# Kernel tuning notes

Hardware: AMD Instinct MI355X
Metric: run time of the kernel (lower is better)

The kernel has to match this reference:

```python
import jax, jax.numpy as jnp
import numpy as np

N_USER = 50000
N_ITEM = 100000
D = 64            # embed_size; layer_size = [64, 64, 64]
NL = 3            # number of propagation layers
NNZ = 2400000     # nonzeros of sparse Laplacian L
B = 1024          # batch of (user, pos_item, neg_item)
N = N_USER + N_ITEM


def setup_inputs() -> dict:
    key = jax.random.key(0)
    ks = jax.random.split(key, 20)
    inp = {}
    # learned parameters
    inp["user_emb"] = jax.random.normal(ks[0], (N_USER, D), jnp.float32) * 0.1
    inp["item_emb"] = jax.random.normal(ks[1], (N_ITEM, D), jnp.float32) * 0.1
    inp["lin1_w"] = jax.random.normal(ks[2], (4, D // 2), jnp.float32) * 0.5
    inp["lin1_b"] = jnp.zeros((D // 2,), jnp.float32)
    inp["lin2_w"] = jax.random.normal(ks[3], (D // 2, D), jnp.float32) * 0.2
    inp["lin2_b"] = jnp.zeros((D,), jnp.float32)
    inp["w1"] = jax.random.normal(ks[4], (NL, D, D), jnp.float32) * (1.0 / np.sqrt(D))
    inp["b1"] = jnp.zeros((NL, D), jnp.float32)
    inp["w2"] = jax.random.normal(ks[5], (NL, D, D), jnp.float32) * (1.0 / np.sqrt(D))
    inp["b2"] = jnp.zeros((NL, D), jnp.float32)
    # sparse normalized Laplacian L in COO form (eye_mat handled as +E)
    inp["lap_row"] = jax.random.randint(ks[6], (NNZ,), 0, N, jnp.int32)
    inp["lap_col"] = jax.random.randint(ks[7], (NNZ,), 0, N, jnp.int32)
    inp["lap_val"] = jax.random.uniform(ks[8], (NNZ,), jnp.float32) * (1.0 / 16.0)
    # forward args
    inp["user_idx"] = jax.random.randint(ks[9], (B,), 0, N_USER, jnp.int32)
    inp["user_feat"] = jax.random.normal(ks[10], (B, 4), jnp.float32)
    inp["pos_idx"] = jax.random.randint(ks[11], (B,), 0, N_ITEM, jnp.int32)
    inp["neg_idx"] = jax.random.randint(ks[12], (B,), 0, N_ITEM, jnp.int32)
    inp["mlp_ratio"] = jnp.float32(0.5)
    return inp


def reference(user_emb, item_emb, user_feat, lin1_w, lin1_b, lin2_w, lin2_b,
              w1, b1, w2, b2, lap_val, mlp_ratio,
              lap_row, lap_col, user_idx, pos_idx, neg_idx):
    n_user = user_emb.shape[0]
    n_nodes = user_emb.shape[0] + item_emb.shape[0]

    # user MLP: two stacked Linears (no activation in between, per Sequential)
    user_mlp = (user_feat @ lin1_w + lin1_b) @ lin2_w + lin2_b  # [B, D]
    # in-place no_grad embedding blend (stop_gradient mirrors torch.no_grad on mlp path)
    upd = user_emb[user_idx] * (1.0 - mlp_ratio) + jax.lax.stop_gradient(user_mlp) * mlp_ratio
    ue = user_emb.at[user_idx].set(upd)

    E = jnp.concatenate([ue, item_emb], axis=0)  # [N, D]

    def spmm(X):
        # L @ X via gather-multiply-segment_sum over COO nonzeros
        return jax.ops.segment_sum(lap_val[:, None] * X[lap_col], lap_row,
                                   num_segments=n_nodes)

    all_E = [E]
    for k in range(w1.shape[0]):
        L_E = spmm(E)                 # L @ E
        L_I_E = L_E + E               # (L + I) @ E
        msg = (L_I_E @ w1[k] + b1[k]) + ((L_E * E) @ w2[k] + b2[k])
        E = jax.nn.leaky_relu(msg, negative_slope=0.2)
        # F.normalize(E, p=2, dim=1) with eps=1e-12
        norm = E / jnp.maximum(jnp.linalg.norm(E, axis=1, keepdims=True), 1e-12)
        all_E.append(norm)

    all_E = jnp.concatenate(all_E, axis=1)  # [N, D*(NL+1)]
    users = all_E[:n_user]
    items = all_E[n_user:]
    return (users[user_idx], items[pos_idx], items[neg_idx])
```

## Files before the change

### kernel.cpp

```cpp
#include <hip/hip_runtime.h>
#include <hip/hip_bf16.h>

#define N_USERC 50000
#define N_ITEMC 100000
#define NNODE   150000
#define DIM     64
#define NLAYERS 3
#define NNZC    2400000
#define BATCH   1024

#define RPB     128
#define NBUCK   1172
#define NCHUNK  512
#define CHUNK   4688
#define CAPB    3072
#define NPARTB  8

using short8 = __attribute__((ext_vector_type(8))) short;
using f32x4  = __attribute__((ext_vector_type(4))) float;
using uintx4 = __attribute__((ext_vector_type(4))) unsigned;

__device__ __forceinline__ float bf2f(ushort u) {
    return __uint_as_float(((unsigned)u) << 16);
}
__device__ __forceinline__ ushort f2bf(float f) {
    unsigned u = __float_as_uint(f);
    u += 0x7FFF + ((u >> 16) & 1);
    return (ushort)(u >> 16);
}

__device__ __forceinline__ int block_excl_scan(int v, int* lds) {
    int lane = threadIdx.x & 63;
    int wid  = threadIdx.x >> 6;
    int nw   = (blockDim.x + 63) >> 6;
    int inc = v;
#pragma unroll
    for (int o = 1; o < 64; o <<= 1) {
        int n = __shfl_up(inc, o, 64);
        if (lane >= o) inc += n;
    }
    if (lane == 63) lds[wid] = inc;
    __syncthreads();
    if (wid == 0) {
        int tv = (lane < nw) ? lds[lane] : 0;
#pragma unroll
        for (int o = 1; o < 16; o <<= 1) {
            int n = __shfl_up(tv, o, 64);
            if (lane >= o) tv += n;
        }
        if (lane < nw) lds[lane] = tv;
    }
    __syncthreads();
    int woff = (wid == 0) ? 0 : lds[wid - 1];
    return woff + (inc - v);
}

__global__ void k_copy_E(const float* __restrict__ ue, const float* __restrict__ ie,
                         ushort* __restrict__ Ebf) {
    int i = blockIdx.x * blockDim.x + threadIdx.x;
    const int userEnd = N_USERC * DIM / 4;
    const int total   = NNODE * DIM / 4;
    if (i < total) {
        float4 v;
        if (i < userEnd) v = ((const float4*)ue)[i];
        else             v = ((const float4*)ie)[i - userEnd];
        ushort4 b;
        b.x = f2bf(v.x); b.y = f2bf(v.y); b.z = f2bf(v.z); b.w = f2bf(v.w);
        ((ushort4*)Ebf)[i] = b;
    }
}

__global__ void k_winner(const int* __restrict__ user_idx, int* __restrict__ winner) {
    int b = blockIdx.x * blockDim.x + threadIdx.x;
    if (b < BATCH) atomicMax(&winner[user_idx[b]], b);
}

__global__ void k_mlp_update(const float* __restrict__ user_emb,
                             const float* __restrict__ user_feat,
                             const float* __restrict__ l1w, const float* __restrict__ l1b,
                             const float* __restrict__ l2w, const float* __restrict__ l2b,
                             const float* __restrict__ ratio_p,
                             const int* __restrict__ user_idx,
                             const int* __restrict__ winner,
                             ushort* __restrict__ Ebf) {
    int b = blockIdx.x;
    int d = threadIdx.x;
    int u = user_idx[b];
    if (winner[u] != b) return;
    float ratio = ratio_p[0];
    float uf0 = user_feat[b * 4 + 0], uf1 = user_feat[b * 4 + 1];
    float uf2 = user_feat[b * 4 + 2], uf3 = user_feat[b * 4 + 3];
    float acc = l2b[d];
#pragma unroll
    for (int j = 0; j < 32; ++j) {
        float h = l1b[j] + uf0 * l1w[0 * 32 + j] + uf1 * l1w[1 * 32 + j]
                         + uf2 * l1w[2 * 32 + j] + uf3 * l1w[3 * 32 + j];
        acc += h * l2w[j * DIM + d];
    }
    float v = user_emb[u * DIM + d] * (1.f - ratio) + acc * ratio;
    Ebf[u * DIM + d] = f2bf(v);
}

__global__ void k_prepW(const float* __restrict__ w1, const float* __restrict__ w2,
                        ushort* __restrict__ Wtg) {
    int i = blockIdx.x * blockDim.x + threadIdx.x;
    if (i >= NLAYERS * 64 * 128) return;
    int layer = i >> 13;
    int rem = i & 8191;
    int n = rem >> 7, kk = rem & 127;
    float v = (kk < 64) ? w1[layer * 4096 + kk * 64 + n]
                        : w2[layer * 4096 + (kk - 64) * 64 + n];
    Wtg[i] = f2bf(v);
}

__global__ __launch_bounds__(256) void k_chunksort(const int* __restrict__ rows,
                                                   const int* __restrict__ cols,
                                                   const float* __restrict__ vals,
                                                   unsigned long long* __restrict__ tmp,
                                                   ushort* __restrict__ scanus) {
    __shared__ int hist[NBUCK];
    __shared__ int sutil[16];
    __shared__ unsigned long long stag[CHUNK];

    const int c = blockIdx.x;
    const int s = c * CHUNK;
    const int e = (s + CHUNK < NNZC) ? s + CHUNK : NNZC;
    const int t = threadIdx.x;

    for (int i = t; i < NBUCK; i += 256) hist[i] = 0;
    __syncthreads();
    for (int i = s + t; i < e; i += 256) atomicAdd(&hist[rows[i] >> 7], 1);
    __syncthreads();

    int loc[5];
    int sum = 0;
#pragma unroll
    for (int k = 0; k < 5; ++k) {
        int idx = t * 5 + k;
        int v = (idx < NBUCK) ? hist[idx] : 0;
        loc[k] = sum;
        sum += v;
    }
    int excl = block_excl_scan(sum, sutil);
#pragma unroll
    for (int k = 0; k < 5; ++k) {
        int idx = t * 5 + k;
        if (idx < NBUCK) hist[idx] = excl + loc[k];
    }
    __syncthreads();

    for (int i = t; i < NBUCK; i += 256) scanus[(size_t)c * (NBUCK + 1) + i] = (ushort)hist[i];
    if (t == 0) scanus[(size_t)c * (NBUCK + 1) + NBUCK] = (ushort)(e - s);
    __syncthreads();

    for (int i = s + t; i < e; i += 256) {
        int r = rows[i];
        int b = r >> 7, ro = r & 127;
        unsigned hi = ((unsigned)ro << 18) | (unsigned)cols[i];
        unsigned long long pk = ((unsigned long long)hi << 32) | (unsigned)__float_as_uint(vals[i]);
        int pos = atomicAdd(&hist[b], 1);
        stag[pos] = pk;
    }
    __syncthreads();

    int n = e - s;
    for (int i = t; i < n; i += 256) tmp[s + i] = stag[i];
}

__global__ __launch_bounds__(256) void k_buckcnt(const ushort* __restrict__ scanus,
                                                 int* __restrict__ bcntp) {
    int b = blockIdx.x * 256 + threadIdx.x;
    int g = blockIdx.y;
    if (b >= NBUCK) return;
    int c0 = g * (NCHUNK / NPARTB), c1 = c0 + NCHUNK / NPARTB;
    int sum = 0;
    for (int c = c0; c < c1; ++c) {
        const ushort* row = scanus + (size_t)c * (NBUCK + 1);
        sum += (int)row[b + 1] - (int)row[b];
    }
    bcntp[g * NBUCK + b] = sum;
}

__global__ __launch_bounds__(256) void k_bscan(const int* __restrict__ bcntp,
                                               int* __restrict__ bstart,
                                               int* __restrict__ rowptr) {
    __shared__ int sutil[16];
    int t = threadIdx.x;
    int loc[5];
    int sum = 0;
#pragma unroll
    for (int k = 0; k < 5; ++k) {
        int idx = t * 5 + k;
        int v = 0;
        if (idx < NBUCK) {
#pragma unroll
            for (int g = 0; g < NPARTB; ++g) v += bcntp[g * NBUCK + idx];
        }
        loc[k] = sum;
        sum += v;
    }
    int excl = block_excl_scan(sum, sutil);
#pragma unroll
    for (int k = 0; k < 5; ++k) {
        int idx = t * 5 + k;
        if (idx < NBUCK) bstart[idx] = excl + loc[k];
    }
    if (t == 0) { bstart[NBUCK] = NNZC; rowptr[NNODE] = NNZC; }
}

__global__ __launch_bounds__(256) void k_compact(const ushort* __restrict__ scanus,
                                                 const int* __restrict__ bstart,
                                                 const unsigned long long* __restrict__ tmp,
                                                 unsigned long long* __restrict__ csr,
                                                 int* __restrict__ rowptr) {
    __shared__ int runstart[NCHUNK];
    __shared__ int pref[NCHUNK + 1];
    __shared__ int sutil[16];
    __shared__ int rcur[RPB];
    __shared__ unsigned long long stag[CAPB];
    const int b = blockIdx.x;
    const int t = threadIdx.x;

    for (int r = t; r < NCHUNK; r += 256) {
        const ushort* row = scanus + (size_t)r * (NBUCK + 1);
        int s0 = row[b], s1 = row[b + 1];
        runstart[r] = r * CHUNK + s0;
        pref[r] = s1 - s0;
    }
    if (t < RPB) rcur[t] = 0;
    __syncthreads();
    int v0 = pref[t * 2], v1 = pref[t * 2 + 1];
    int sum = v0 + v1;
    int excl = block_excl_scan(sum, sutil);
    pref[t * 2] = excl;
    pref[t * 2 + 1] = excl + v0;
    if (t == 255) pref[NCHUNK] = excl + sum;
    __syncthreads();

    const int total = pref[NCHUNK];
    const int obase = bstart[b];

    if (total <= CAPB) {
        for (int r = t; r < NCHUNK; r += 256) {
            int p0 = pref[r], p1 = pref[r + 1];
            int rs = runstart[r];
            for (int i = p0; i < p1; ++i) stag[i] = tmp[rs + (i - p0)];
        }
        __syncthreads();
        for (int i = t; i < total; i += 256)
            atomicAdd(&rcur[(int)(stag[i] >> 50) & 127], 1);
        __syncthreads();
        int rv = (t < RPB) ? rcur[t] : 0;
        int rex = block_excl_scan(rv, sutil);
        if (t < RPB) {
            rcur[t] = rex;
            int grow = b * RPB + t;
            if (grow < NNODE) rowptr[grow] = obase + rex;
        }
        __syncthreads();
        for (int i = t; i < total; i += 256) {
            unsigned long long pk = stag[i];
            int ro = (int)(pk >> 50) & 127;
            int pos = atomicAdd(&rcur[ro], 1);
            csr[obase + pos] = pk;
        }
        return;
    }

    for (int i = t; i < total; i += 256) {
        int lo = 0, hi = NCHUNK - 1;
        while (lo < hi) {
            int mid = (lo + hi + 1) >> 1;
            if (pref[mid] <= i) lo = mid; else hi = mid - 1;
        }
        unsigned long long pk = tmp[runstart[lo] + (i - pref[lo])];
        atomicAdd(&rcur[(int)(pk >> 50) & 127], 1);
    }
    __syncthreads();
    int rv = (t < RPB) ? rcur[t] : 0;
    int rex = block_excl_scan(rv, sutil);
    if (t < RPB) {
        rcur[t] = rex;
        int grow = b * RPB + t;
        if (grow < NNODE) rowptr[grow] = obase + rex;
    }
    __syncthreads();
    for (int i = t; i < total; i += 256) {
        int lo = 0, hi = NCHUNK - 1;
        while (lo < hi) {
            int mid = (lo + hi + 1) >> 1;
            if (pref[mid] <= i) lo = mid; else hi = mid - 1;
        }
        unsigned long long pk = tmp[runstart[lo] + (i - pref[lo])];
        int ro = (int)(pk >> 50) & 127;
        int pos = atomicAdd(&rcur[ro], 1);
        csr[obase + pos] = pk;
    }
}

__device__ __forceinline__ float gacc16c(const unsigned long long* __restrict__ csr,
                                         const ushort* __restrict__ Ep, int j, int m) {
    unsigned long long pk[16];
    float ev[16];
#pragma unroll
    for (int k = 0; k < 16; ++k) pk[k] = csr[j + k];
#pragma unroll
    for (int k = 0; k < 16; ++k) {
        int col = (k < m) ? ((int)(pk[k] >> 32) & 0x3FFFF) : 0;
        ev[k] = bf2f(Ep[col * DIM]);
    }
    float a = 0.f;
#pragma unroll
    for (int k = 0; k < 16; ++k) {
        unsigned v = (k < m) ? (unsigned)pk[k] : 0u;
        a += __uint_as_float(v) * ev[k];
    }
    return a;
}

__global__ __launch_bounds__(256) void k_spmm(const int* __restrict__ rowptr,
                                              const unsigned long long* __restrict__ csr,
                                              const ushort* __restrict__ Ebf,
                                              ushort* __restrict__ Abf) {
    int lane = threadIdx.x & 63;
    int pair = blockIdx.x * 4 + (threadIdx.x >> 6);
    pair = __builtin_amdgcn_readfirstlane(pair);
    int rowA = pair * 2;
    if (rowA >= NNODE) return;
    int rowB = rowA + 1;
    int sA = __builtin_amdgcn_readfirstlane(rowptr[rowA]);
    int eA = __builtin_amdgcn_readfirstlane(rowptr[rowA + 1]);
    int eB = __builtin_amdgcn_readfirstlane(rowptr[rowA + 2]);
    const ushort* Ep = Ebf + lane;
    float eoA = bf2f(Ebf[rowA * DIM + lane]);
    float eoB = bf2f(Ebf[rowB * DIM + lane]);
    int nrA = (eA - sA + 15) >> 4;
    int nrB = (eB - eA + 15) >> 4;
    int rmax = nrA > nrB ? nrA : nrB;
    int jA = sA, jB = eA;
    float accA = 0.f, accB = 0.f;
    for (int r = 0; r < rmax; ++r) {
        accA += gacc16c(csr, Ep, jA, eA - jA); jA += 16;
        accB += gacc16c(csr, Ep, jB, eB - jB); jB += 16;
    }
    __builtin_nontemporal_store(f2bf(accA + eoA), &Abf[rowA * 128 + lane]);
    __builtin_nontemporal_store(f2bf(accA * eoA), &Abf[rowA * 128 + 64 + lane]);
    __builtin_nontemporal_store(f2bf(accB + eoB), &Abf[rowB * 128 + lane]);
    __builtin_nontemporal_store(f2bf(accB * eoB), &Abf[rowB * 128 + 64 + lane]);
}

__global__ __launch_bounds__(256) void k_transform(const ushort* __restrict__ Abf,
                                                   const ushort* __restrict__ Wtg,
                                                   const float* __restrict__ b1k,
                                                   const float* __restrict__ b2k,
                                                   ushort* __restrict__ Ebf_out) {
    __shared__ ushort A_s[64 * 136];
    __shared__ ushort W_s[64 * 136];
    __shared__ float  bias_s[64];

    const int t = threadIdx.x;
    const int rowbase = blockIdx.x * 64;
    if (t < 64) bias_s[t] = b1k[t] + b2k[t];

#pragma unroll
    for (int it = 0; it < 4; ++it) {
        int task = t + 256 * it;
        int n = task >> 4, k = (task & 15) * 8;
        uint4 wv = *(const uint4*)&Wtg[n * 128 + k];
        *(uint4*)&W_s[n * 136 + k] = wv;
    }
#pragma unroll
    for (int it = 0; it < 4; ++it) {
        int task = t + 256 * it;
        int rl = task >> 4, k8 = (task & 15) * 8;
        int row = rowbase + rl;
        uintx4 v = {0u, 0u, 0u, 0u};
        if (row < NNODE)
            v = __builtin_nontemporal_load((const uintx4*)&Abf[row * 128 + k8]);
        *(uintx4*)&A_s[rl * 136 + k8] = v;
    }
    __syncthreads();

    const int w = t >> 6, l = t & 63;
    const int m16 = l & 15;
    const int q   = l >> 4;
    const int lm  = w * 16 + m16;

    f32x4 z = {0.f, 0.f, 0.f, 0.f};
    f32x4 acc[4] = {z, z, z, z};
#pragma unroll
    for (int ks = 0; ks < 4; ++ks) {
        short8 af = *(const short8*)&A_s[lm * 136 + ks * 32 + q * 8];
#pragma unroll
        for (int nt = 0; nt < 4; ++nt) {
            short8 wf = *(const short8*)&W_s[(nt * 16 + m16) * 136 + ks * 32 + q * 8];
            acc[nt] = __builtin_amdgcn_mfma_f32_16x16x32_bf16(af, wf, acc[nt], 0, 0, 0);
        }
    }
    __syncthreads();

    float* Cs = (float*)A_s;
#pragma unroll
    for (int nt = 0; nt < 4; ++nt) {
        int col = nt * 16 + m16;
#pragma unroll
        for (int r = 0; r < 4; ++r) {
            int lrow = w * 16 + q * 4 + r;
            Cs[lrow * 68 + col] = acc[nt][r];
        }
    }
    __syncthreads();

#pragma unroll
    for (int it = 0; it < 2; ++it) {
        int task = t + 256 * it;
        int rl = task >> 3, col = (task & 7) * 8;
        int row = rowbase + rl;
        if (row < NNODE) {
            float4 v0 = *(const float4*)&Cs[rl * 68 + col];
            float4 v1 = *(const float4*)&Cs[rl * 68 + col + 4];
            float o[8] = {v0.x, v0.y, v0.z, v0.w, v1.x, v1.y, v1.z, v1.w};
            ushort ob[8];
#pragma unroll
            for (int j = 0; j < 8; ++j) {
                float v = o[j] + bias_s[col + j];
                v = v >= 0.f ? v : 0.2f * v;
                ob[j] = f2bf(v);
            }
            uint4 pb;
            pb.x = (unsigned)ob[0] | ((unsigned)ob[1] << 16);
            pb.y = (unsigned)ob[2] | ((unsigned)ob[3] << 16);
            pb.z = (unsigned)ob[4] | ((unsigned)ob[5] << 16);
            pb.w = (unsigned)ob[6] | ((unsigned)ob[7] << 16);
            *(uint4*)&Ebf_out[row * 64 + col] = pb;
        }
    }
}

__global__ __launch_bounds__(256) void k_gather(const ushort* __restrict__ Ebf,
                                                const int* __restrict__ user_idx,
                                                const int* __restrict__ pos_idx,
                                                const int* __restrict__ neg_idx,
                                                float* __restrict__ out,
                                                int seg, int normalize) {
    int wid  = threadIdx.x >> 6;
    int lane = threadIdx.x & 63;
    int o = blockIdx.x * 4 + wid;
    if (o >= 3 * BATCH) return;
    int g = o >> 10, b = o & 1023;
    int row;
    if (g == 0)      row = user_idx[b];
    else if (g == 1) row = N_USERC + pos_idx[b];
    else             row = N_USERC + neg_idx[b];
    float v = bf2f(Ebf[row * DIM + lane]);
    if (normalize) {
        float ss = v * v;
#pragma unroll
        for (int m = 32; m; m >>= 1) ss += __shfl_xor(ss, m, 64);
        float nrm = sqrtf(ss);
        nrm = fmaxf(nrm, 1e-12f);
        v = v / nrm;
    }
    out[(g * BATCH + b) * 256 + seg * 64 + lane] = v;
}

extern "C" void kernel_launch(void* const* d_in, const int* in_sizes, int n_in,
                              void* d_out, int out_size, void* d_ws, size_t ws_size,
                              hipStream_t stream) {
    const float* user_emb  = (const float*)d_in[0];
    const float* item_emb  = (const float*)d_in[1];
    const float* lin1_w    = (const float*)d_in[2];
    const float* lin1_b    = (const float*)d_in[3];
    const float* lin2_w    = (const float*)d_in[4];
    const float* lin2_b    = (const float*)d_in[5];
    const float* w1        = (const float*)d_in[6];
    const float* b1        = (const float*)d_in[7];
    const float* w2        = (const float*)d_in[8];
    const float* b2        = (const float*)d_in[9];
    const int*   lap_row   = (const int*)d_in[10];
    const int*   lap_col   = (const int*)d_in[11];
    const float* lap_val   = (const float*)d_in[12];
    const int*   user_idx  = (const int*)d_in[13];
    const float* user_feat = (const float*)d_in[14];
    const int*   pos_idx   = (const int*)d_in[15];
    const int*   neg_idx   = (const int*)d_in[16];
    const float* mlp_ratio = (const float*)d_in[17];
    float* out = (float*)d_out;

    size_t off = 0;
    auto carve = [&](size_t bytes) { size_t r = off; off = (off + bytes + 255) & ~(size_t)255; return r; };
    size_t oL      = carve((size_t)NNODE * DIM * 4);
    size_t oEbf    = carve((size_t)NNODE * DIM * 2);
    size_t oCsr    = carve((size_t)NNZC * 8);
    size_t oScan   = carve((size_t)NCHUNK * (NBUCK + 1) * 2);
    size_t oBcnt   = carve((size_t)NBUCK * 4);
    size_t oBstart = carve((size_t)(NBUCK + 1) * 4);
    size_t oRowptr = carve((size_t)(NNODE + 1) * 4);
    size_t oWinner = carve((size_t)N_USERC * 4);
    size_t oBcntP  = carve((size_t)NPARTB * NBUCK * 4);
    (void)ws_size; (void)oBcnt;

    char* base = (char*)d_ws;
    ushort*             Abf    = (ushort*)(base + oL);
    unsigned long long* tmp    = (unsigned long long*)(base + oL);
    ushort*             Ebf    = (ushort*)(base + oEbf);
    unsigned long long* csr    = (unsigned long long*)(base + oCsr);
    ushort*             scanus = (ushort*)(base + oScan);
    int*                bstart = (int*)(base + oBstart);
    int*                rowptr = (int*)(base + oRowptr);
    int*                winner = (int*)(base + oWinner);
    int*                bcntp  = (int*)(base + oBcntP);
    ushort*             Wtg    = (ushort*)(base + oScan);

    k_chunksort<<<NCHUNK, 256, 0, stream>>>(lap_row, lap_col, lap_val, tmp, scanus);
    k_buckcnt<<<dim3(5, NPARTB), 256, 0, stream>>>(scanus, bcntp);
    k_bscan<<<1, 256, 0, stream>>>(bcntp, bstart, rowptr);
    k_compact<<<NBUCK, 256, 0, stream>>>(scanus, bstart, tmp, csr, rowptr);

    k_prepW<<<(NLAYERS * 64 * 128 + 255) / 256, 256, 0, stream>>>(w1, w2, Wtg);
    hipMemsetAsync(winner, 0xFF, (size_t)N_USERC * 4, stream);
    k_copy_E<<<(NNODE * DIM / 4 + 255) / 256, 256, 0, stream>>>(user_emb, item_emb, Ebf);
    k_winner<<<(BATCH + 255) / 256, 256, 0, stream>>>(user_idx, winner);
    k_mlp_update<<<BATCH, 64, 0, stream>>>(user_emb, user_feat, lin1_w, lin1_b,
                                           lin2_w, lin2_b, mlp_ratio, user_idx, winner, Ebf);
    k_gather<<<(3 * BATCH) / 4, 256, 0, stream>>>(Ebf, user_idx, pos_idx, neg_idx, out, 0, 0);

    for (int k = 0; k < NLAYERS; ++k) {
        k_spmm<<<(NNODE / 2 + 3) / 4, 256, 0, stream>>>(rowptr, csr, Ebf, Abf);
        k_transform<<<(NNODE + 63) / 64, 256, 0, stream>>>(
            Abf, Wtg + (size_t)k * 64 * 128, b1 + (size_t)k * DIM,
            b2 + (size_t)k * DIM, Ebf);
        k_gather<<<(3 * BATCH) / 4, 256, 0, stream>>>(Ebf, user_idx, pos_idx, neg_idx,
                                                      out, k + 1, 1);
    }
}
```

Baseline: 443.8 us.

## Fuse SpMM and dense transform into one per-layer kernel with ping-pong buffers

Replaces the separate k_spmm and k_transform kernels with a single k_layer kernel. Each wave computes the SpMM results for 16 rows directly into LDS, then runs the MFMA transform with weights read straight from global memory. Output goes to an alternate E buffer (ping-pong) because rows are now read and written in the same kernel. This removes the global write and re-read of the intermediate bf16 [N,128] buffer and one launch per layer. In exchange, each wave gathers its rows one at a time instead of interleaving two, which gives less memory-level parallelism.

```diff
diff --git a/kernel.cpp b/kernel.cpp
--- a/kernel.cpp
+++ b/kernel.cpp
@@ -318,86 +318,57 @@
     return a;
 }
 
-__global__ __launch_bounds__(256) void k_spmm(const int* __restrict__ rowptr,
-                                              const unsigned long long* __restrict__ csr,
-                                              const ushort* __restrict__ Ebf,
-                                              ushort* __restrict__ Abf) {
-    int lane = threadIdx.x & 63;
-    int pair = blockIdx.x * 4 + (threadIdx.x >> 6);
-    pair = __builtin_amdgcn_readfirstlane(pair);
-    int rowA = pair * 2;
-    if (rowA >= NNODE) return;
-    int rowB = rowA + 1;
-    int sA = __builtin_amdgcn_readfirstlane(rowptr[rowA]);
-    int eA = __builtin_amdgcn_readfirstlane(rowptr[rowA + 1]);
-    int eB = __builtin_amdgcn_readfirstlane(rowptr[rowA + 2]);
-    const ushort* Ep = Ebf + lane;
-    float eoA = bf2f(Ebf[rowA * DIM + lane]);
-    float eoB = bf2f(Ebf[rowB * DIM + lane]);
-    int nrA = (eA - sA + 15) >> 4;
-    int nrB = (eB - eA + 15) >> 4;
-    int rmax = nrA > nrB ? nrA : nrB;
-    int jA = sA, jB = eA;
-    float accA = 0.f, accB = 0.f;
-    for (int r = 0; r < rmax; ++r) {
-        accA += gacc16c(csr, Ep, jA, eA - jA); jA += 16;
-        accB += gacc16c(csr, Ep, jB, eB - jB); jB += 16;
-    }
-    __builtin_nontemporal_store(f2bf(accA + eoA), &Abf[rowA * 128 + lane]);
-    __builtin_nontemporal_store(f2bf(accA * eoA), &Abf[rowA * 128 + 64 + lane]);
-    __builtin_nontemporal_store(f2bf(accB + eoB), &Abf[rowB * 128 + lane]);
-    __builtin_nontemporal_store(f2bf(accB * eoB), &Abf[rowB * 128 + 64 + lane]);
-}
-
-__global__ __launch_bounds__(256) void k_transform(const ushort* __restrict__ Abf,
-                                                   const ushort* __restrict__ Wtg,
-                                                   const float* __restrict__ b1k,
-                                                   const float* __restrict__ b2k,
-                                                   ushort* __restrict__ Ebf_out) {
+__global__ __launch_bounds__(256) void k_layer(const int* __restrict__ rowptr,
+                                               const unsigned long long* __restrict__ csr,
+                                               const ushort* __restrict__ Ein,
+                                               const ushort* __restrict__ Wtg,
+                                               const float* __restrict__ b1k,
+                                               const float* __restrict__ b2k,
+                                               ushort* __restrict__ Eout) {
     __shared__ ushort A_s[64 * 136];
-    __shared__ ushort W_s[64 * 136];
     __shared__ float  bias_s[64];
 
     const int t = threadIdx.x;
+    const int w = t >> 6, lane = t & 63;
     const int rowbase = blockIdx.x * 64;
     if (t < 64) bias_s[t] = b1k[t] + b2k[t];
 
-#pragma unroll
-    for (int it = 0; it < 4; ++it) {
-        int task = t + 256 * it;
-        int n = task >> 4, k = (task & 15) * 8;
-        uint4 wv = *(const uint4*)&Wtg[n * 128 + k];
-        *(uint4*)&W_s[n * 136 + k] = wv;
-    }
-#pragma unroll
-    for (int it = 0; it < 4; ++it) {
-        int task = t + 256 * it;
-        int rl = task >> 4, k8 = (task & 15) * 8;
-        int row = rowbase + rl;
-        uintx4 v = {0u, 0u, 0u, 0u};
-        if (row < NNODE)
-            v = __builtin_nontemporal_load((const uintx4*)&Abf[row * 128 + k8]);
-        *(uintx4*)&A_s[rl * 136 + k8] = v;
-    }
-    __syncthreads();
-
-    const int w = t >> 6, l = t & 63;
-    const int m16 = l & 15;
-    const int q   = l >> 4;
+    const ushort* Ep = Ein + lane;
+
+    for (int rr = 0; rr < 16; ++rr) {
+        int lr = w * 16 + rr;
+        int row = rowbase + lr;
+        float accP = 0.f, accM = 0.f;
+        if (row < NNODE) {
+            int s = __builtin_amdgcn_readfirstlane(rowptr[row]);
+            int e = __builtin_amdgcn_readfirstlane(rowptr[row + 1]);
+            float eo = bf2f(Ein[row * DIM + lane]);
+            float acc = 0.f;
+            int j = s;
+            for (; j + 16 <= e; j += 16) acc += gacc16c(csr, Ep, j, 16);
+            if (j < e) acc += gacc16c(csr, Ep, j, e - j);
+            accP = acc + eo;
+            accM = acc * eo;
+        }
+        A_s[lr * 136 + lane]      = f2bf(accP);
+        A_s[lr * 136 + 64 + lane] = f2bf(accM);
+    }
+
+    const int m16 = lane & 15;
+    const int q   = lane >> 4;
     const int lm  = w * 16 + m16;
 
     f32x4 z = {0.f, 0.f, 0.f, 0.f};
-    f32x4 acc[4] = {z, z, z, z};
+    f32x4 acc4[4] = {z, z, z, z};
 #pragma unroll
     for (int ks = 0; ks < 4; ++ks) {
         short8 af = *(const short8*)&A_s[lm * 136 + ks * 32 + q * 8];
 #pragma unroll
         for (int nt = 0; nt < 4; ++nt) {
-            short8 wf = *(const short8*)&W_s[(nt * 16 + m16) * 136 + ks * 32 + q * 8];
-            acc[nt] = __builtin_amdgcn_mfma_f32_16x16x32_bf16(af, wf, acc[nt], 0, 0, 0);
-        }
-    }
-    __syncthreads();
+            short8 wf = *(const short8*)&Wtg[(nt * 16 + m16) * 128 + ks * 32 + q * 8];
+            acc4[nt] = __builtin_amdgcn_mfma_f32_16x16x32_bf16(af, wf, acc4[nt], 0, 0, 0);
+        }
+    }
 
     float* Cs = (float*)A_s;
 #pragma unroll
@@ -406,7 +377,7 @@
 #pragma unroll
         for (int r = 0; r < 4; ++r) {
             int lrow = w * 16 + q * 4 + r;
-            Cs[lrow * 68 + col] = acc[nt][r];
+            Cs[lrow * 68 + col] = acc4[nt][r];
         }
     }
     __syncthreads();
@@ -432,7 +403,7 @@
             pb.y = (unsigned)ob[2] | ((unsigned)ob[3] << 16);
             pb.z = (unsigned)ob[4] | ((unsigned)ob[5] << 16);
             pb.w = (unsigned)ob[6] | ((unsigned)ob[7] << 16);
-            *(uint4*)&Ebf_out[row * 64 + col] = pb;
+            *(uint4*)&Eout[row * 64 + col] = pb;
         }
     }
 }
@@ -501,8 +472,8 @@
     (void)ws_size; (void)oBcnt;
 
     char* base = (char*)d_ws;
-    ushort*             Abf    = (ushort*)(base + oL);
     unsigned long long* tmp    = (unsigned long long*)(base + oL);
+    ushort*             Epong  = (ushort*)(base + oL);
     ushort*             Ebf    = (ushort*)(base + oEbf);
     unsigned long long* csr    = (unsigned long long*)(base + oCsr);
     ushort*             scanus = (ushort*)(base + oScan);
@@ -525,12 +496,14 @@
                                            lin2_w, lin2_b, mlp_ratio, user_idx, winner, Ebf);
     k_gather<<<(3 * BATCH) / 4, 256, 0, stream>>>(Ebf, user_idx, pos_idx, neg_idx, out, 0, 0);
 
+    ushort* Ecur = Ebf;
     for (int k = 0; k < NLAYERS; ++k) {
-        k_spmm<<<(NNODE / 2 + 3) / 4, 256, 0, stream>>>(rowptr, csr, Ebf, Abf);
-        k_transform<<<(NNODE + 63) / 64, 256, 0, stream>>>(
-            Abf, Wtg + (size_t)k * 64 * 128, b1 + (size_t)k * DIM,
-            b2 + (size_t)k * DIM, Ebf);
-        k_gather<<<(3 * BATCH) / 4, 256, 0, stream>>>(Ebf, user_idx, pos_idx, neg_idx,
+        ushort* Enext = (Ecur == Ebf) ? Epong : Ebf;
+        k_layer<<<(NNODE + 63) / 64, 256, 0, stream>>>(
+            rowptr, csr, Ecur, Wtg + (size_t)k * 64 * 128,
+            b1 + (size_t)k * DIM, b2 + (size_t)k * DIM, Enext);
+        k_gather<<<(3 * BATCH) / 4, 256, 0, stream>>>(Enext, user_idx, pos_idx, neg_idx,
                                                       out, k + 1, 1);
-    }
-}
+        Ecur = Enext;
+    }
+}
```

Result: faster. 430.9 us (-2.9%).
